# Performance work log

Measured on AMD Instinct MI355X. Metric: run time of the kernel, lower is better.

## Reference

```python
import jax, jax.numpy as jnp
import numpy as np

B, S, IN_D, OUT_D, QD = 4, 1024, 16, 16, 32
HID, HEADS, HD, L, TED = 256, 8, 32, 4, 256
DECAY = 0.1
SCALE = HD ** -0.5


def _ln(x):
    m = x.mean(-1, keepdims=True)
    v = ((x - m) ** 2).mean(-1, keepdims=True)
    return (x - m) * jax.lax.rsqrt(v + 1e-5)


def _lin(x, w, b):
    # torch nn.Linear: y = x @ W^T + b, W is [out, in]
    return jnp.einsum('...i,oi->...o', x, w) + b


def _sin_emb(t, dim):
    half = dim // 2
    freqs = jnp.exp(-np.log(10000.0) * jnp.arange(half, dtype=jnp.float32) / (half - 1))
    a = t[:, None] * freqs[None, :]
    return jnp.concatenate([jnp.sin(a), jnp.cos(a)], axis=-1)


def _mish(x):
    return x * jnp.tanh(jax.nn.softplus(x))


def _gelu(x):
    return jax.nn.gelu(x, approximate=False)


def setup_inputs() -> dict:
    key = jax.random.key(0)
    ks = iter(jax.random.split(key, 64))

    def w(shape):
        return jax.random.normal(next(ks), shape, dtype=jnp.float32) * 0.02

    d = {}
    d['x'] = jax.random.normal(next(ks), (B, S, IN_D), dtype=jnp.float32)
    d['query'] = jax.random.normal(next(ks), (B, QD), dtype=jnp.float32)
    d['time'] = jax.random.uniform(next(ks), (B,), dtype=jnp.float32) * 1000.0
    d['tm_w1'] = w((TED * 4, TED)); d['tm_b1'] = jnp.zeros((TED * 4,), jnp.float32)
    d['tm_w2'] = w((TED, TED * 4)); d['tm_b2'] = jnp.zeros((TED,), jnp.float32)
    d['in_w'] = w((HID, IN_D)); d['in_b'] = jnp.zeros((HID,), jnp.float32)
    d['q_w1'] = w((HID, QD)); d['q_b1'] = jnp.zeros((HID,), jnp.float32)
    d['q_w2'] = w((HID, HID)); d['q_b2'] = jnp.zeros((HID,), jnp.float32)
    d['n1_w'] = jnp.ones((L, HID), jnp.float32); d['n1_b'] = jnp.zeros((L, HID), jnp.float32)
    d['qkv_w'] = w((L, 3 * HID, HID)); d['qkv_b'] = jnp.zeros((L, 3 * HID), jnp.float32)
    d['ap_w'] = w((L, HID, HID)); d['ap_b'] = jnp.zeros((L, HID), jnp.float32)
    d['rel_bias'] = w((L, 2 * S - 1, HEADS))
    d['n2_w'] = jnp.ones((L, HID), jnp.float32); d['n2_b'] = jnp.zeros((L, HID), jnp.float32)
    d['f1_w'] = w((L, 4 * HID, HID)); d['f1_b'] = jnp.zeros((L, 4 * HID), jnp.float32)
    d['f2_w'] = w((L, HID, 4 * HID)); d['f2_b'] = jnp.zeros((L, HID), jnp.float32)
    d['t1_w'] = w((L, HID, TED)); d['t1_b'] = jnp.zeros((L, HID), jnp.float32)
    d['t2_w'] = w((L, HID, HID)); d['t2_b'] = jnp.zeros((L, HID), jnp.float32)
    d['out_w'] = w((OUT_D, HID)); d['out_b'] = jnp.zeros((OUT_D,), jnp.float32)
    return d


def reference(x, query, time, tm_w1, tm_b1, tm_w2, tm_b2, in_w, in_b,
              q_w1, q_b1, q_w2, q_b2, n1_w, n1_b, qkv_w, qkv_b, ap_w, ap_b,
              rel_bias, n2_w, n2_b, f1_w, f1_b, f2_w, f2_b, t1_w, t1_b,
              t2_w, t2_b, out_w, out_b):
    Bx, Sx, _ = x.shape
    # time MLP: SinusoidalPosEmb -> Linear -> Mish -> Linear
    te = _lin(_sin_emb(time, TED), tm_w1, tm_b1)
    te = _lin(_mish(te), tm_w2, tm_b2)            # [B, TED]
    # input projection + query conditioning (relative-pos path: no abs pos emb)
    h = _lin(x, in_w, in_b)                        # [B, S, HID]
    qe = _lin(_gelu(_lin(query, q_w1, q_b1)), q_w2, q_b2)
    h = h + qe[:, None, :]
    # shared relative-distance structures
    idx = jnp.arange(Sx)
    rel = idx[:, None] - idx[None, :]              # [S, S]
    dec = jnp.exp(-DECAY * jnp.abs(rel).astype(jnp.float32))
    rel_idx = rel + S - 1                          # index into 2*max_seq_len-1 table
    for l in range(L):
        # time conditioning per block
        tp = _lin(_gelu(_lin(te, t1_w[l], t1_b[l])), t2_w[l], t2_b[l])
        xn = _ln(h + tp[:, None, :]) * n1_w[l] + n1_b[l]
        qkv = _lin(xn, qkv_w[l], qkv_b[l]).reshape(Bx, Sx, 3, HEADS, HD)
        qkv = qkv.transpose(2, 0, 3, 1, 4)          # [3, B, H, S, hd]
        q_, k_, v_ = qkv[0], qkv[1], qkv[2]
        attn = jnp.einsum('bhqd,bhkd->bhqk', q_, k_) * SCALE
        bias = rel_bias[l][rel_idx]                 # [S, S, H]
        attn = attn + (dec[:, :, None] * bias).transpose(2, 0, 1)[None]
        a = jax.nn.softmax(attn, axis=-1)
        o = jnp.einsum('bhqk,bhkd->bhqd', a, v_)
        o = o.transpose(0, 2, 1, 3).reshape(Bx, Sx, HID)
        h = h + _lin(o, ap_w[l], ap_b[l])           # residual from pre-time x
        xn2 = _ln(h) * n2_w[l] + n2_b[l]
        h = h + _lin(_gelu(_lin(xn2, f1_w[l], f1_b[l])), f2_w[l], f2_b[l])
    return _lin(h, out_w, out_b)
```

## Files before the change

kernel.cpp:

```cpp
#include <hip/hip_runtime.h>
#include <hip/hip_bf16.h>
#include <math.h>

#define S_LEN 1024
#define HID 256
#define HEADS 8
#define HD 32
#define NLAYER 4
#define TED 256
#define BATCH 4
#define DECAY 0.1f
#define ATT_SCALE 0.17677669529663687f
#define LOG2E 1.4426950408889634f

typedef __bf16 bf8_t __attribute__((ext_vector_type(8)));
typedef float f4_t __attribute__((ext_vector_type(4)));

__device__ __forceinline__ float gelu_f(float x) {
  return 0.5f * x * (1.f + erff(x * 0.70710678118654752f));
}
__device__ __forceinline__ __bf16 f2bf(float f) { return (__bf16)f; }

__global__ __launch_bounds__(256) void k_prep_a(
    const float* __restrict__ timev,
    const float* __restrict__ tm_w1, const float* __restrict__ tm_b1,
    const float* __restrict__ query,
    const float* __restrict__ q_w1, const float* __restrict__ q_b1,
    float* __restrict__ te1, float* __restrict__ q1) {
  int bid = blockIdx.x;
  int lane = threadIdx.x & 63;
  if (bid < 1024) {
    int r = bid * 4 + (threadIdx.x >> 6);
    int o = r & 1023, b = r >> 10;
    float t = timev[b];
    float ev[4];
#pragma unroll
    for (int e = 0; e < 4; e++) {
      int k = lane * 4 + e;
      int i = k & 127;
      float f = __expf(-logf(10000.f) * (float)i / 127.f);
      float a = t * f;
      ev[e] = (k < 128) ? sinf(a) : cosf(a);
    }
    const float* w = tm_w1 + (size_t)o * 256 + lane * 4;
    float4 w4 = *(const float4*)w;
    float s = ev[0] * w4.x + ev[1] * w4.y + ev[2] * w4.z + ev[3] * w4.w;
#pragma unroll
    for (int off = 32; off; off >>= 1) s += __shfl_xor(s, off);
    if (lane == 0) {
      s += tm_b1[o];
      float sp = (s > 20.f) ? s : log1pf(__expf(s));
      te1[r] = s * tanhf(sp);
    }
  } else {
    int r = (bid - 1024) * 4 + (threadIdx.x >> 6);
    int o = r & 255, b = r >> 8;
    float s = 0.f;
    if (lane < 8) {
      float4 a4 = *(const float4*)(query + b * 32 + lane * 4);
      float4 w4 = *(const float4*)(q_w1 + (size_t)o * 32 + lane * 4);
      s = a4.x * w4.x + a4.y * w4.y + a4.z * w4.z + a4.w * w4.w;
    }
#pragma unroll
    for (int off = 32; off; off >>= 1) s += __shfl_xor(s, off);
    if (lane == 0) q1[r] = gelu_f(s + q_b1[o]);
  }
}

__global__ __launch_bounds__(256) void k_prep_b(
    const float* __restrict__ te1, const float* __restrict__ tm_w2,
    const float* __restrict__ tm_b2,
    const float* __restrict__ q1, const float* __restrict__ q_w2,
    const float* __restrict__ q_b2,
    float* __restrict__ te, float* __restrict__ qe) {
  int bid = blockIdx.x;
  int lane = threadIdx.x & 63;
  bool iste = bid < 256;
  int r = (iste ? bid : bid - 256) * 4 + (threadIdx.x >> 6);
  int o = r & 255, b = r >> 8;
  int K = iste ? 1024 : 256;
  const float* a = (iste ? te1 : q1) + (size_t)b * K;
  const float* w = (iste ? tm_w2 : q_w2) + (size_t)o * K;
  float s = 0.f;
  for (int k = lane * 4; k < K; k += 256) {
    float4 a4 = *(const float4*)(a + k);
    float4 w4 = *(const float4*)(w + k);
    s += a4.x * w4.x + a4.y * w4.y + a4.z * w4.z + a4.w * w4.w;
  }
#pragma unroll
  for (int off = 32; off; off >>= 1) s += __shfl_xor(s, off);
  if (lane == 0) {
    s += (iste ? tm_b2 : q_b2)[o];
    (iste ? te : qe)[r] = s;
  }
}

template <int ACT, bool APG>
__global__ __launch_bounds__(256) void k_gemv(
    const float* __restrict__ A, const float* __restrict__ W,
    const float* __restrict__ bias, float* __restrict__ out,
    int K, int OUT) {
  int r = blockIdx.x * 4 + (threadIdx.x >> 6);
  int lane = threadIdx.x & 63;
  int o = r % OUT;
  int b = (r / OUT) % BATCH;
  int g = r / (OUT * BATCH);
  const float* a = A + (size_t)((APG ? g * BATCH : 0) + b) * K;
  const float* w = W + (size_t)(g * OUT + o) * K;
  float s = 0.f;
  for (int k = lane * 4; k < K; k += 256) {
    float4 a4 = *(const float4*)(a + k);
    float4 w4 = *(const float4*)(w + k);
    s += a4.x * w4.x + a4.y * w4.y + a4.z * w4.z + a4.w * w4.w;
  }
#pragma unroll
  for (int off = 32; off; off >>= 1) s += __shfl_xor(s, off);
  if (lane == 0) {
    s += bias[g * OUT + o];
    if (ACT == 1) s = gelu_f(s);
    if (ACT == 2) {
      float sp = (s > 20.f) ? s : log1pf(__expf(s));
      s = s * tanhf(sp);
    }
    out[r] = s;
  }
}

__global__ __launch_bounds__(256) void k_inproj(
    const float* __restrict__ x, const float* __restrict__ in_w,
    const float* __restrict__ in_b, const float* __restrict__ qe,
    float* __restrict__ h) {
  int row = blockIdx.x;
  int b = row >> 10;
  int j = threadIdx.x;
  __shared__ float xr[16];
  if (j < 16) xr[j] = x[row * 16 + j];
  __syncthreads();
  float s = in_b[j] + qe[b * 256 + j];
  const float* w = in_w + j * 16;
#pragma unroll
  for (int i = 0; i < 16; i++) s += xr[i] * w[i];
  h[(size_t)row * 256 + j] = s;
}

__global__ __launch_bounds__(256) void k_cvtall(
    const float* __restrict__ s0, __bf16* __restrict__ d0,
    const float* __restrict__ s1, __bf16* __restrict__ d1,
    const float* __restrict__ s2, __bf16* __restrict__ d2,
    const float* __restrict__ s3, __bf16* __restrict__ d3,
    const float* __restrict__ relb, float* __restrict__ decb_t) {
  int bid = blockIdx.x;
  if (bid >= 1536) {
    int lb = bid - 1536;
    int l = lb >> 6;
    int i = (lb & 63) * 256 + threadIdx.x;
    if (i < 2047 * 8) {
      int idx = i >> 3, hh = i & 7;
      float dec = __expf(-DECAY * fabsf((float)(idx - 1023)));
      decb_t[(l * 8 + hh) * 2048 + idx] = dec * relb[(size_t)l * 2047 * 8 + i] * LOG2E;
    }
    return;
  }
  const float* s; __bf16* d; int base;
  if (bid < 384)       { s = s0; d = d0; base = bid; }
  else if (bid < 512)  { s = s1; d = d1; base = bid - 384; }
  else if (bid < 1024) { s = s2; d = d2; base = bid - 512; }
  else                 { s = s3; d = d3; base = bid - 1024; }
  int i = (base * 256 + threadIdx.x) * 8;
  float4 a = *(const float4*)(s + i);
  float4 b = *(const float4*)(s + i + 4);
  bf8_t o;
  o[0] = f2bf(a.x); o[1] = f2bf(a.y); o[2] = f2bf(a.z); o[3] = f2bf(a.w);
  o[4] = f2bf(b.x); o[5] = f2bf(b.y); o[6] = f2bf(b.z); o[7] = f2bf(b.w);
  *(bf8_t*)(d + i) = o;
}

template <int BN, int ACT, int OUTMODE, bool HASTP>
__global__ __launch_bounds__(256) void k_gemm_lnf(
    const float* __restrict__ h, const __bf16* __restrict__ W,
    const float* __restrict__ bias, void* __restrict__ Cv,
    const float* __restrict__ tp, const float* __restrict__ lw,
    const float* __restrict__ lb, int N) {
  constexpr int K = 256;
  constexpr int NJ = (BN / 2) / 16;
  constexpr int BQ = BN / 64;
  __shared__ __bf16 Al[64 * 264];
  __shared__ __bf16 Bl[2 * BN * 32];
  int tid = threadIdx.x;
  int w = tid >> 6, lane = tid & 63;
  int g = lane >> 4, c = lane & 15;
  int n0 = blockIdx.x * BN, m0 = blockIdx.y * 64;

  int srow = tid >> 2;
  int scol = (tid & 3) * 8;
  int sw = (((tid & 3) ^ ((tid >> 3) & 3))) * 8;
  const __bf16* Wb = W + (size_t)n0 * K + scol;
  bf8_t nB[2][BQ];
#pragma unroll
  for (int sub = 0; sub < 2; sub++)
#pragma unroll
    for (int q = 0; q < BQ; q++)
      nB[sub][q] = *(const bf8_t*)(Wb + (size_t)(q * 64 + srow) * K + sub * 32);

  int sub32 = tid & 31, lrow = tid >> 5;
  int colb = sub32 * 8;
  float4 lw0 = *(const float4*)(lw + colb), lw1 = *(const float4*)(lw + colb + 4);
  float4 lb0 = *(const float4*)(lb + colb), lb1 = *(const float4*)(lb + colb + 4);
  float4 tp0, tp1;
  if (HASTP) {
    const float* tpr = tp + (m0 >> 10) * 256 + colb;
    tp0 = *(const float4*)tpr; tp1 = *(const float4*)(tpr + 4);
  }
#pragma unroll
  for (int p = 0; p < 8; p++) {
    int row = p * 8 + lrow;
    const float* hr = h + (size_t)(m0 + row) * 256 + colb;
    float4 a = *(const float4*)hr;
    float4 b2 = *(const float4*)(hr + 4);
    if (HASTP) {
      a.x += tp0.x; a.y += tp0.y; a.z += tp0.z; a.w += tp0.w;
      b2.x += tp1.x; b2.y += tp1.y; b2.z += tp1.z; b2.w += tp1.w;
    }
    float sum = a.x + a.y + a.z + a.w + b2.x + b2.y + b2.z + b2.w;
    float ss = a.x * a.x + a.y * a.y + a.z * a.z + a.w * a.w +
               b2.x * b2.x + b2.y * b2.y + b2.z * b2.z + b2.w * b2.w;
#pragma unroll
    for (int m = 1; m < 32; m <<= 1) {
      sum += __shfl_xor(sum, m);
      ss += __shfl_xor(ss, m);
    }
    float mean = sum * (1.f / 256.f);
    float var = ss * (1.f / 256.f) - mean * mean;
    float rs = rsqrtf(var + 1e-5f);
    bf8_t o;
    o[0] = f2bf((a.x - mean) * rs * lw0.x + lb0.x);
    o[1] = f2bf((a.y - mean) * rs * lw0.y + lb0.y);
    o[2] = f2bf((a.z - mean) * rs * lw0.z + lb0.z);
    o[3] = f2bf((a.w - mean) * rs * lw0.w + lb0.w);
    o[4] = f2bf((b2.x - mean) * rs * lw1.x + lb1.x);
    o[5] = f2bf((b2.y - mean) * rs * lw1.y + lb1.y);
    o[6] = f2bf((b2.z - mean) * rs * lw1.z + lb1.z);
    o[7] = f2bf((b2.w - mean) * rs * lw1.w + lb1.w);
    *(bf8_t*)&Al[row * 264 + colb] = o;
  }

  int wr = (w >> 1) * 32, wc = (w & 1) * (BN / 2);
  int aseg = ((g ^ ((c >> 1) & 3))) * 8;
  f4_t acc[2][NJ];
#pragma unroll
  for (int i = 0; i < 2; i++)
#pragma unroll
    for (int j = 0; j < NJ; j++) acc[i][j] = (f4_t){0.f, 0.f, 0.f, 0.f};

#pragma unroll
  for (int ph = 0; ph < 4; ph++) {
    __syncthreads();
#pragma unroll
    for (int sub = 0; sub < 2; sub++)
#pragma unroll
      for (int q = 0; q < BQ; q++)
        *(bf8_t*)&Bl[sub * BN * 32 + (q * 64 + srow) * 32 + sw] = nB[sub][q];
    __syncthreads();
    if (ph < 3) {
#pragma unroll
      for (int sub = 0; sub < 2; sub++)
#pragma unroll
        for (int q = 0; q < BQ; q++)
          nB[sub][q] = *(const bf8_t*)(Wb + (size_t)(q * 64 + srow) * K +
                                       (ph + 1) * 64 + sub * 32);
    }
#pragma unroll
    for (int sub = 0; sub < 2; sub++) {
      bf8_t af[2], bfr[NJ];
#pragma unroll
      for (int i = 0; i < 2; i++)
        af[i] = *(const bf8_t*)&Al[(wr + i * 16 + c) * 264 + ph * 64 + sub * 32 + g * 8];
#pragma unroll
      for (int j = 0; j < NJ; j++)
        bfr[j] = *(const bf8_t*)&Bl[sub * BN * 32 + (wc + j * 16 + c) * 32 + aseg];
#pragma unroll
      for (int i = 0; i < 2; i++)
#pragma unroll
        for (int j = 0; j < NJ; j++)
          acc[i][j] = __builtin_amdgcn_mfma_f32_16x16x32_bf16(af[i], bfr[j], acc[i][j], 0, 0, 0);
    }
  }
#pragma unroll
  for (int j = 0; j < NJ; j++) {
    int col = n0 + wc + j * 16 + c;
    float bv = bias[col];
#pragma unroll
    for (int i = 0; i < 2; i++) {
#pragma unroll
      for (int rr = 0; rr < 4; rr++) {
        int row = m0 + wr + i * 16 + 4 * g + rr;
        float v = acc[i][j][rr] + bv;
        if (ACT == 1) v = gelu_f(v);
        size_t idx = (size_t)row * N + col;
        if (OUTMODE == 1) ((float*)Cv)[idx] += v;
        else ((__bf16*)Cv)[idx] = f2bf(v);
      }
    }
  }
}

__global__ __launch_bounds__(256) void k_attn(
    const __bf16* __restrict__ qkv, const float* __restrict__ decb_t,
    __bf16* __restrict__ obuf) {
  __shared__ __bf16 Kl[64 * 40];
  __shared__ __bf16 Vt[32 * 72];
  __shared__ __bf16 Pl[4][16 * 72];
  __shared__ float db[1088];

  int tid = threadIdx.x;
  int w = tid >> 6, lane = tid & 63;
  int g = lane >> 4, c = lane & 15;
  int bh = blockIdx.y;
  int b = bh >> 3, hh = bh & 7;
  int q0 = blockIdx.x * 64;

  for (int i = tid; i < 1087; i += 256) db[i] = decb_t[hh * 2048 + q0 + i];

  bf8_t qraw = *(const bf8_t*)(qkv + ((size_t)(b * S_LEN + q0 + w * 16 + c)) * 768 + hh * 32 + 8 * g);
  bf8_t qfrag;
#pragma unroll
  for (int i = 0; i < 8; i++) qfrag[i] = f2bf((float)qraw[i] * (ATT_SCALE * LOG2E));

  float ps_acc[4] = {0.f, 0.f, 0.f, 0.f};
  f4_t o0 = {0.f, 0.f, 0.f, 0.f}, o1 = {0.f, 0.f, 0.f, 0.f};

  int rowb = w * 16 + 4 * g;
  __bf16* Plw = &Pl[w][0];

  int kvr = tid & 63, part = tid >> 6;
  const __bf16* base0 = qkv + ((size_t)(b * S_LEN + kvr)) * 768 + hh * 32 + part * 8;
  bf8_t k8 = *(const bf8_t*)(base0 + 256);
  bf8_t v8 = *(const bf8_t*)(base0 + 512);

  for (int c0 = 0; c0 < S_LEN; c0 += 64) {
    __syncthreads();
    {
      *(bf8_t*)&Kl[kvr * 40 + part * 8] = k8;
      int d0s = part * 8;
#pragma unroll
      for (int jj = 0; jj < 8; jj++) Vt[(d0s + jj) * 72 + kvr] = v8[jj];
    }
    __syncthreads();
    if (c0 + 64 < S_LEN) {
      const __bf16* basen = base0 + (size_t)(c0 + 64) * 768;
      k8 = *(const bf8_t*)(basen + 256);
      v8 = *(const bf8_t*)(basen + 512);
    }

    f4_t sc[4];
    f4_t zero4 = {0.f, 0.f, 0.f, 0.f};
#pragma unroll
    for (int j = 0; j < 4; j++) {
      bf8_t kfrag = *(const bf8_t*)&Kl[(j * 16 + c) * 40 + g * 8];
      sc[j] = __builtin_amdgcn_mfma_f32_16x16x32_bf16(qfrag, kfrag, zero4, 0, 0, 0);
    }
#pragma unroll
    for (int j = 0; j < 4; j++) {
      int bidx = rowb + 1023 - (c0 + j * 16 + c);
#pragma unroll
      for (int r = 0; r < 4; r++) {
        float p = exp2f(sc[j][r] + db[bidx + r]);
        ps_acc[r] += p;
        Plw[(4 * g + r) * 72 + j * 16 + c] = f2bf(p);
      }
    }
#pragma unroll
    for (int ss = 0; ss < 2; ss++) {
      bf8_t pa = *(const bf8_t*)&Plw[c * 72 + ss * 32 + g * 8];
      bf8_t v0 = *(const bf8_t*)&Vt[c * 72 + ss * 32 + g * 8];
      bf8_t v1 = *(const bf8_t*)&Vt[(c + 16) * 72 + ss * 32 + g * 8];
      o0 = __builtin_amdgcn_mfma_f32_16x16x32_bf16(pa, v0, o0, 0, 0, 0);
      o1 = __builtin_amdgcn_mfma_f32_16x16x32_bf16(pa, v1, o1, 0, 0, 0);
    }
  }

#pragma unroll
  for (int r = 0; r < 4; r++) {
#pragma unroll
    for (int m = 1; m < 16; m <<= 1) ps_acc[r] += __shfl_xor(ps_acc[r], m);
    float inv = 1.f / ps_acc[r];
    size_t rowg = (size_t)(b * S_LEN + q0 + rowb + r);
    obuf[rowg * 256 + hh * 32 + c] = f2bf(o0[r] * inv);
    obuf[rowg * 256 + hh * 32 + 16 + c] = f2bf(o1[r] * inv);
  }
}

__global__ __launch_bounds__(512) void k_back(
    const __bf16* __restrict__ obb, float* __restrict__ h,
    const __bf16* __restrict__ wap, const float* __restrict__ apb,
    const float* __restrict__ n2w, const float* __restrict__ n2b,
    const __bf16* __restrict__ wf1, const float* __restrict__ f1b,
    const __bf16* __restrict__ wf2, const float* __restrict__ f2b) {
  __shared__ __bf16 Asm[16 * 264];
  __shared__ __bf16 Bl[2 * 256 * 32];
  __shared__ __bf16 y1l[16 * 1032];
  __shared__ float red[16][8][2];

  int tid = threadIdx.x;
  int w = tid >> 6, lane = tid & 63;
  int g = lane >> 4, c = lane & 15;
  int m0 = blockIdx.x * 16;
  int srow = tid >> 2;
  int scol = (tid & 3) * 8;
  int sw = (((tid & 3) ^ ((srow >> 1) & 3))) * 8;
  int wc = w * 32;
  int axor = (c >> 1) & 3;
  int boff0 = (wc + c) * 32 + ((g ^ axor)) * 8;
  int boff1 = (wc + 16 + c) * 32 + ((g ^ axor)) * 8;
  int col0 = wc + c, col1 = wc + 16 + c;
  f4_t zero4 = {0.f, 0.f, 0.f, 0.f};

  bf8_t nB[2][2];
  auto prefetch = [&](const __bf16* base, int K, int ko) {
#pragma unroll
    for (int s = 0; s < 2; s++)
#pragma unroll
      for (int q = 0; q < 2; q++)
        nB[s][q] = *(const bf8_t*)(base + (size_t)(q * 128 + srow) * K + ko + s * 32 + scol);
  };
  auto stageB = [&]() {
    __syncthreads();
#pragma unroll
    for (int s = 0; s < 2; s++)
#pragma unroll
      for (int q = 0; q < 2; q++)
        *(bf8_t*)&Bl[s * 8192 + (q * 128 + srow) * 32 + sw] = nB[s][q];
    __syncthreads();
  };
  f4_t a0, a1;
  auto mstep = [&](const __bf16* Ab, int AS, int ko) {
#pragma unroll
    for (int s = 0; s < 2; s++) {
      bf8_t af = *(const bf8_t*)&Ab[c * AS + ko + s * 32 + g * 8];
      bf8_t b0 = *(const bf8_t*)&Bl[s * 8192 + boff0];
      bf8_t b1 = *(const bf8_t*)&Bl[s * 8192 + boff1];
      a0 = __builtin_amdgcn_mfma_f32_16x16x32_bf16(af, b0, a0, 0, 0, 0);
      a1 = __builtin_amdgcn_mfma_f32_16x16x32_bf16(af, b1, a1, 0, 0, 0);
    }
  };

  prefetch(wap, 256, 0);
  {
    int row = tid >> 5, gr = tid & 31;
    *(bf8_t*)&Asm[row * 264 + gr * 8] = *(const bf8_t*)(obb + (size_t)(m0 + row) * 256 + gr * 8);
  }

  a0 = zero4; a1 = zero4;
#pragma unroll
  for (int ph = 0; ph < 4; ph++) {
    stageB();
    if (ph < 3) prefetch(wap, 256, (ph + 1) * 64);
    else prefetch(wf1, 256, 0);
    mstep(Asm, 264, ph * 64);
  }

  float hn[2][4];
  {
    float b0v = apb[col0], b1v = apb[col1];
    float ps[4], pq[4];
#pragma unroll
    for (int r = 0; r < 4; r++) {
      size_t row = (size_t)(m0 + 4 * g + r);
      float v0 = a0[r] + b0v + h[row * 256 + col0];
      float v1 = a1[r] + b1v + h[row * 256 + col1];
      h[row * 256 + col0] = v0;
      h[row * 256 + col1] = v1;
      hn[0][r] = v0; hn[1][r] = v1;
      ps[r] = v0 + v1;
      pq[r] = v0 * v0 + v1 * v1;
    }
#pragma unroll
    for (int r = 0; r < 4; r++) {
#pragma unroll
      for (int m = 1; m < 16; m <<= 1) {
        ps[r] += __shfl_xor(ps[r], m);
        pq[r] += __shfl_xor(pq[r], m);
      }
    }
    if (c == 0) {
#pragma unroll
      for (int r = 0; r < 4; r++) {
        red[4 * g + r][w][0] = ps[r];
        red[4 * g + r][w][1] = pq[r];
      }
    }
  }
  __syncthreads();
  {
    float n2w0 = n2w[col0], n2b0 = n2b[col0];
    float n2w1 = n2w[col1], n2b1 = n2b[col1];
#pragma unroll
    for (int r = 0; r < 4; r++) {
      int row = 4 * g + r;
      float S = 0.f, Q = 0.f;
#pragma unroll
      for (int ww = 0; ww < 8; ww++) { S += red[row][ww][0]; Q += red[row][ww][1]; }
      float mean = S * (1.f / 256.f);
      float var = Q * (1.f / 256.f) - mean * mean;
      float rs = rsqrtf(var + 1e-5f);
      Asm[row * 264 + col0] = f2bf((hn[0][r] - mean) * rs * n2w0 + n2b0);
      Asm[row * 264 + col1] = f2bf((hn[1][r] - mean) * rs * n2w1 + n2b1);
    }
  }

#pragma unroll
  for (int nc = 0; nc < 4; nc++) {
    a0 = zero4; a1 = zero4;
#pragma unroll
    for (int ph = 0; ph < 4; ph++) {
      stageB();
      if (ph < 3) prefetch(wf1 + nc * 65536, 256, (ph + 1) * 64);
      else if (nc < 3) prefetch(wf1 + (nc + 1) * 65536, 256, 0);
      else prefetch(wf2, 1024, 0);
      mstep(Asm, 264, ph * 64);
    }
    float b0v = f1b[nc * 256 + col0], b1v = f1b[nc * 256 + col1];
#pragma unroll
    for (int r = 0; r < 4; r++) {
      y1l[(4 * g + r) * 1032 + nc * 256 + col0] = f2bf(gelu_f(a0[r] + b0v));
      y1l[(4 * g + r) * 1032 + nc * 256 + col1] = f2bf(gelu_f(a1[r] + b1v));
    }
  }

  a0 = zero4; a1 = zero4;
#pragma unroll
  for (int ph = 0; ph < 16; ph++) {
    stageB();
    if (ph < 15) prefetch(wf2, 1024, (ph + 1) * 64);
    mstep(y1l, 1032, ph * 64);
  }
  {
    float b0v = f2b[col0], b1v = f2b[col1];
#pragma unroll
    for (int r = 0; r < 4; r++) {
      size_t row = (size_t)(m0 + 4 * g + r);
      h[row * 256 + col0] += a0[r] + b0v;
      h[row * 256 + col1] += a1[r] + b1v;
    }
  }
}

__global__ __launch_bounds__(256) void k_out(
    const float* __restrict__ hbuf, const float* __restrict__ out_w,
    const float* __restrict__ out_b, float* __restrict__ out) {
  int tid = threadIdx.x;
  int r = blockIdx.x * 16 + (tid >> 4);
  int c = tid & 15;
  const float4* hr = (const float4*)(hbuf + (size_t)r * 256);
  const float4* w4 = (const float4*)(out_w + c * 256);
  float s = out_b[c];
#pragma unroll 8
  for (int k = 0; k < 64; k++) {
    float4 a = hr[k], b = w4[k];
    s += a.x * b.x + a.y * b.y + a.z * b.z + a.w * b.w;
  }
  out[r * 16 + c] = s;
}

extern "C" void kernel_launch(void* const* d_in, const int* in_sizes, int n_in,
                              void* d_out, int out_size, void* d_ws, size_t ws_size,
                              hipStream_t stream) {
  const float* x      = (const float*)d_in[0];
  const float* query  = (const float*)d_in[1];
  const float* timev  = (const float*)d_in[2];
  const float* tm_w1  = (const float*)d_in[3];
  const float* tm_b1  = (const float*)d_in[4];
  const float* tm_w2  = (const float*)d_in[5];
  const float* tm_b2  = (const float*)d_in[6];
  const float* in_w   = (const float*)d_in[7];
  const float* in_b   = (const float*)d_in[8];
  const float* q_w1   = (const float*)d_in[9];
  const float* q_b1   = (const float*)d_in[10];
  const float* q_w2   = (const float*)d_in[11];
  const float* q_b2   = (const float*)d_in[12];
  const float* n1_w   = (const float*)d_in[13];
  const float* n1_b   = (const float*)d_in[14];
  const float* qkv_w  = (const float*)d_in[15];
  const float* qkv_b  = (const float*)d_in[16];
  const float* ap_w   = (const float*)d_in[17];
  const float* ap_b   = (const float*)d_in[18];
  const float* relb   = (const float*)d_in[19];
  const float* n2_w   = (const float*)d_in[20];
  const float* n2_b   = (const float*)d_in[21];
  const float* f1_w   = (const float*)d_in[22];
  const float* f1_b   = (const float*)d_in[23];
  const float* f2_w   = (const float*)d_in[24];
  const float* f2_b   = (const float*)d_in[25];
  const float* t1_w   = (const float*)d_in[26];
  const float* t1_b   = (const float*)d_in[27];
  const float* t2_w   = (const float*)d_in[28];
  const float* t2_b   = (const float*)d_in[29];
  const float* out_w  = (const float*)d_in[30];
  const float* out_b  = (const float*)d_in[31];
  float* out = (float*)d_out;

  float* ws = (float*)d_ws;
  float*  h    = ws;
  __bf16* qkvb = (__bf16*)(ws + 1572864);
  __bf16* obb  = (__bf16*)(ws + 3145728);
  __bf16* wqkv = (__bf16*)(ws + 5767168);
  __bf16* wap  = (__bf16*)(ws + 6160384);
  __bf16* wf1  = (__bf16*)(ws + 6291456);
  __bf16* wf2  = (__bf16*)(ws + 6815744);
  float* decb  = ws + 7340032;
  float* qe    = decb + 65536;
  float* tp    = qe + 1024;
  float* te1   = tp + 4096;
  float* te    = te1 + 4096;
  float* q1    = te + 1024;
  float* tt    = q1 + 1024;

  k_cvtall<<<1792, 256, 0, stream>>>(qkv_w, wqkv, ap_w, wap, f1_w, wf1, f2_w, wf2,
                                     relb, decb);

  k_prep_a<<<1280, 256, 0, stream>>>(timev, tm_w1, tm_b1, query, q_w1, q_b1, te1, q1);
  k_prep_b<<<512, 256, 0, stream>>>(te1, tm_w2, tm_b2, q1, q_w2, q_b2, te, qe);
  k_gemv<1, false><<<1024, 256, 0, stream>>>(te, t1_w, t1_b, tt, 256, 256);
  k_gemv<0, true><<<1024, 256, 0, stream>>>(tt, t2_w, t2_b, tp, 256, 256);

  k_inproj<<<4096, 256, 0, stream>>>(x, in_w, in_b, qe, h);

  for (int l = 0; l < NLAYER; l++) {
    k_gemm_lnf<128, 0, 2, true><<<dim3(6, 64), 256, 0, stream>>>(
        h, wqkv + (size_t)l * 196608, qkv_b + l * 768, qkvb,
        tp + l * 1024, n1_w + l * 256, n1_b + l * 256, 768);
    k_attn<<<dim3(16, 32), 256, 0, stream>>>(qkvb, decb + l * 16384, obb);
    k_back<<<256, 512, 0, stream>>>(
        obb, h, wap + (size_t)l * 65536, ap_b + l * 256,
        n2_w + l * 256, n2_b + l * 256,
        wf1 + (size_t)l * 262144, f1_b + l * 1024,
        wf2 + (size_t)l * 262144, f2_b + l * 256);
  }
  k_out<<<256, 256, 0, stream>>>(h, out_w, out_b, out);
}
```

Before: 282.7 us.

## Widen attention KV tile to 128, add MFMA priority hints, merge prep kernels

The attention kernel now processes 128 keys per iteration instead of 64. This halves the number of barrier-synchronised tile loads and doubles the MFMA work done between syncs, and s_setprio raises wave priority around the MFMA sections. Separately, the weight-conversion and first prep kernels are merged into one launch, as are the time-MLP first GEMV and the input projection, which removes launch overhead. The larger tiles raise LDS use (Kl, Vt, Pl) and register pressure from sc[8], which may reduce occupancy.

```diff
diff --git a/kernel.cpp b/kernel.cpp
--- a/kernel.cpp
+++ b/kernel.cpp
@@ -21,7 +21,12 @@
 }
 __device__ __forceinline__ __bf16 f2bf(float f) { return (__bf16)f; }
 
-__global__ __launch_bounds__(256) void k_prep_a(
+__global__ __launch_bounds__(256) void k_boot(
+    const float* __restrict__ s0, __bf16* __restrict__ d0,
+    const float* __restrict__ s1, __bf16* __restrict__ d1,
+    const float* __restrict__ s2, __bf16* __restrict__ d2,
+    const float* __restrict__ s3, __bf16* __restrict__ d3,
+    const float* __restrict__ relb, float* __restrict__ decb_t,
     const float* __restrict__ timev,
     const float* __restrict__ tm_w1, const float* __restrict__ tm_b1,
     const float* __restrict__ query,
@@ -29,8 +34,30 @@
     float* __restrict__ te1, float* __restrict__ q1) {
   int bid = blockIdx.x;
   int lane = threadIdx.x & 63;
-  if (bid < 1024) {
-    int r = bid * 4 + (threadIdx.x >> 6);
+  if (bid < 1536) {
+    const float* s; __bf16* d; int base;
+    if (bid < 384)       { s = s0; d = d0; base = bid; }
+    else if (bid < 512)  { s = s1; d = d1; base = bid - 384; }
+    else if (bid < 1024) { s = s2; d = d2; base = bid - 512; }
+    else                 { s = s3; d = d3; base = bid - 1024; }
+    int i = (base * 256 + threadIdx.x) * 8;
+    float4 a = *(const float4*)(s + i);
+    float4 b = *(const float4*)(s + i + 4);
+    bf8_t o;
+    o[0] = f2bf(a.x); o[1] = f2bf(a.y); o[2] = f2bf(a.z); o[3] = f2bf(a.w);
+    o[4] = f2bf(b.x); o[5] = f2bf(b.y); o[6] = f2bf(b.z); o[7] = f2bf(b.w);
+    *(bf8_t*)(d + i) = o;
+  } else if (bid < 1792) {
+    int lb = bid - 1536;
+    int l = lb >> 6;
+    int i = (lb & 63) * 256 + threadIdx.x;
+    if (i < 2047 * 8) {
+      int idx = i >> 3, hh = i & 7;
+      float dec = __expf(-DECAY * fabsf((float)(idx - 1023)));
+      decb_t[(l * 8 + hh) * 2048 + idx] = dec * relb[(size_t)l * 2047 * 8 + i] * LOG2E;
+    }
+  } else if (bid < 2816) {
+    int r = (bid - 1792) * 4 + (threadIdx.x >> 6);
     int o = r & 1023, b = r >> 10;
     float t = timev[b];
     float ev[4];
@@ -42,8 +69,7 @@
       float a = t * f;
       ev[e] = (k < 128) ? sinf(a) : cosf(a);
     }
-    const float* w = tm_w1 + (size_t)o * 256 + lane * 4;
-    float4 w4 = *(const float4*)w;
+    float4 w4 = *(const float4*)(tm_w1 + (size_t)o * 256 + lane * 4);
     float s = ev[0] * w4.x + ev[1] * w4.y + ev[2] * w4.z + ev[3] * w4.w;
 #pragma unroll
     for (int off = 32; off; off >>= 1) s += __shfl_xor(s, off);
@@ -53,7 +79,7 @@
       te1[r] = s * tanhf(sp);
     }
   } else {
-    int r = (bid - 1024) * 4 + (threadIdx.x >> 6);
+    int r = (bid - 2816) * 4 + (threadIdx.x >> 6);
     int o = r & 255, b = r >> 8;
     float s = 0.f;
     if (lane < 8) {
@@ -95,6 +121,45 @@
   }
 }
 
+__global__ __launch_bounds__(256) void k_mid(
+    const float* __restrict__ te, const float* __restrict__ t1_w,
+    const float* __restrict__ t1_b, float* __restrict__ tt,
+    const float* __restrict__ x, const float* __restrict__ in_w,
+    const float* __restrict__ in_b, const float* __restrict__ qe,
+    float* __restrict__ h) {
+  int bid = blockIdx.x;
+  if (bid < 1024) {
+    int r = bid * 4 + (threadIdx.x >> 6);
+    int lane = threadIdx.x & 63;
+    int o = r & 255;
+    int b = (r >> 8) & 3;
+    int g = r >> 10;
+    const float* a = te + (size_t)b * 256;
+    const float* w = t1_w + ((size_t)(g * 256 + o)) * 256;
+    float s = 0.f;
+    for (int k = lane * 4; k < 256; k += 256) {
+      float4 a4 = *(const float4*)(a + k);
+      float4 w4 = *(const float4*)(w + k);
+      s += a4.x * w4.x + a4.y * w4.y + a4.z * w4.z + a4.w * w4.w;
+    }
+#pragma unroll
+    for (int off = 32; off; off >>= 1) s += __shfl_xor(s, off);
+    if (lane == 0) tt[r] = gelu_f(s + t1_b[g * 256 + o]);
+  } else {
+    int row = bid - 1024;
+    int b = row >> 10;
+    int j = threadIdx.x;
+    __shared__ float xr[16];
+    if (j < 16) xr[j] = x[row * 16 + j];
+    __syncthreads();
+    float s = in_b[j] + qe[b * 256 + j];
+    const float* w = in_w + j * 16;
+#pragma unroll
+    for (int i = 0; i < 16; i++) s += xr[i] * w[i];
+    h[(size_t)row * 256 + j] = s;
+  }
+}
+
 template <int ACT, bool APG>
 __global__ __launch_bounds__(256) void k_gemv(
     const float* __restrict__ A, const float* __restrict__ W,
@@ -126,55 +191,6 @@
   }
 }
 
-__global__ __launch_bounds__(256) void k_inproj(
-    const float* __restrict__ x, const float* __restrict__ in_w,
-    const float* __restrict__ in_b, const float* __restrict__ qe,
-    float* __restrict__ h) {
-  int row = blockIdx.x;
-  int b = row >> 10;
-  int j = threadIdx.x;
-  __shared__ float xr[16];
-  if (j < 16) xr[j] = x[row * 16 + j];
-  __syncthreads();
-  float s = in_b[j] + qe[b * 256 + j];
-  const float* w = in_w + j * 16;
-#pragma unroll
-  for (int i = 0; i < 16; i++) s += xr[i] * w[i];
-  h[(size_t)row * 256 + j] = s;
-}
-
-__global__ __launch_bounds__(256) void k_cvtall(
-    const float* __restrict__ s0, __bf16* __restrict__ d0,
-    const float* __restrict__ s1, __bf16* __restrict__ d1,
-    const float* __restrict__ s2, __bf16* __restrict__ d2,
-    const float* __restrict__ s3, __bf16* __restrict__ d3,
-    const float* __restrict__ relb, float* __restrict__ decb_t) {
-  int bid = blockIdx.x;
-  if (bid >= 1536) {
-    int lb = bid - 1536;
-    int l = lb >> 6;
-    int i = (lb & 63) * 256 + threadIdx.x;
-    if (i < 2047 * 8) {
-      int idx = i >> 3, hh = i & 7;
-      float dec = __expf(-DECAY * fabsf((float)(idx - 1023)));
-      decb_t[(l * 8 + hh) * 2048 + idx] = dec * relb[(size_t)l * 2047 * 8 + i] * LOG2E;
-    }
-    return;
-  }
-  const float* s; __bf16* d; int base;
-  if (bid < 384)       { s = s0; d = d0; base = bid; }
-  else if (bid < 512)  { s = s1; d = d1; base = bid - 384; }
-  else if (bid < 1024) { s = s2; d = d2; base = bid - 512; }
-  else                 { s = s3; d = d3; base = bid - 1024; }
-  int i = (base * 256 + threadIdx.x) * 8;
-  float4 a = *(const float4*)(s + i);
-  float4 b = *(const float4*)(s + i + 4);
-  bf8_t o;
-  o[0] = f2bf(a.x); o[1] = f2bf(a.y); o[2] = f2bf(a.z); o[3] = f2bf(a.w);
-  o[4] = f2bf(b.x); o[5] = f2bf(b.y); o[6] = f2bf(b.z); o[7] = f2bf(b.w);
-  *(bf8_t*)(d + i) = o;
-}
-
 template <int BN, int ACT, int OUTMODE, bool HASTP>
 __global__ __launch_bounds__(256) void k_gemm_lnf(
     const float* __restrict__ h, const __bf16* __restrict__ W,
@@ -307,9 +323,9 @@
 __global__ __launch_bounds__(256) void k_attn(
     const __bf16* __restrict__ qkv, const float* __restrict__ decb_t,
     __bf16* __restrict__ obuf) {
-  __shared__ __bf16 Kl[64 * 40];
-  __shared__ __bf16 Vt[32 * 72];
-  __shared__ __bf16 Pl[4][16 * 72];
+  __shared__ __bf16 Kl[128 * 40];
+  __shared__ __bf16 Vt[32 * 136];
+  __shared__ __bf16 Pl[4][16 * 136];
   __shared__ float db[1088];
 
   int tid = threadIdx.x;
@@ -332,51 +348,63 @@
   int rowb = w * 16 + 4 * g;
   __bf16* Plw = &Pl[w][0];
 
-  int kvr = tid & 63, part = tid >> 6;
-  const __bf16* base0 = qkv + ((size_t)(b * S_LEN + kvr)) * 768 + hh * 32 + part * 8;
-  bf8_t k8 = *(const bf8_t*)(base0 + 256);
-  bf8_t v8 = *(const bf8_t*)(base0 + 512);
-
-  for (int c0 = 0; c0 < S_LEN; c0 += 64) {
+  int kvr = tid & 127;
+  int part = tid >> 7;
+  const __bf16* base0 = qkv + ((size_t)(b * S_LEN + kvr)) * 768 + hh * 32 + part * 16;
+  bf8_t k8a = *(const bf8_t*)(base0 + 256);
+  bf8_t k8b = *(const bf8_t*)(base0 + 264);
+  bf8_t v8a = *(const bf8_t*)(base0 + 512);
+  bf8_t v8b = *(const bf8_t*)(base0 + 520);
+
+  for (int c0 = 0; c0 < S_LEN; c0 += 128) {
     __syncthreads();
     {
-      *(bf8_t*)&Kl[kvr * 40 + part * 8] = k8;
-      int d0s = part * 8;
-#pragma unroll
-      for (int jj = 0; jj < 8; jj++) Vt[(d0s + jj) * 72 + kvr] = v8[jj];
+      *(bf8_t*)&Kl[kvr * 40 + part * 16] = k8a;
+      *(bf8_t*)&Kl[kvr * 40 + part * 16 + 8] = k8b;
+      int d0s = part * 16;
+#pragma unroll
+      for (int jj = 0; jj < 8; jj++) Vt[(d0s + jj) * 136 + kvr] = v8a[jj];
+#pragma unroll
+      for (int jj = 0; jj < 8; jj++) Vt[(d0s + 8 + jj) * 136 + kvr] = v8b[jj];
     }
     __syncthreads();
-    if (c0 + 64 < S_LEN) {
-      const __bf16* basen = base0 + (size_t)(c0 + 64) * 768;
-      k8 = *(const bf8_t*)(basen + 256);
-      v8 = *(const bf8_t*)(basen + 512);
-    }
-
-    f4_t sc[4];
+    if (c0 + 128 < S_LEN) {
+      const __bf16* basen = base0 + (size_t)(c0 + 128) * 768;
+      k8a = *(const bf8_t*)(basen + 256);
+      k8b = *(const bf8_t*)(basen + 264);
+      v8a = *(const bf8_t*)(basen + 512);
+      v8b = *(const bf8_t*)(basen + 520);
+    }
+
+    f4_t sc[8];
     f4_t zero4 = {0.f, 0.f, 0.f, 0.f};
-#pragma unroll
-    for (int j = 0; j < 4; j++) {
+    __builtin_amdgcn_s_setprio(1);
+#pragma unroll
+    for (int j = 0; j < 8; j++) {
       bf8_t kfrag = *(const bf8_t*)&Kl[(j * 16 + c) * 40 + g * 8];
       sc[j] = __builtin_amdgcn_mfma_f32_16x16x32_bf16(qfrag, kfrag, zero4, 0, 0, 0);
     }
-#pragma unroll
-    for (int j = 0; j < 4; j++) {
+    __builtin_amdgcn_s_setprio(0);
+#pragma unroll
+    for (int j = 0; j < 8; j++) {
       int bidx = rowb + 1023 - (c0 + j * 16 + c);
 #pragma unroll
       for (int r = 0; r < 4; r++) {
         float p = exp2f(sc[j][r] + db[bidx + r]);
         ps_acc[r] += p;
-        Plw[(4 * g + r) * 72 + j * 16 + c] = f2bf(p);
+        Plw[(4 * g + r) * 136 + j * 16 + c] = f2bf(p);
       }
     }
-#pragma unroll
-    for (int ss = 0; ss < 2; ss++) {
-      bf8_t pa = *(const bf8_t*)&Plw[c * 72 + ss * 32 + g * 8];
-      bf8_t v0 = *(const bf8_t*)&Vt[c * 72 + ss * 32 + g * 8];
-      bf8_t v1 = *(const bf8_t*)&Vt[(c + 16) * 72 + ss * 32 + g * 8];
+    __builtin_amdgcn_s_setprio(1);
+#pragma unroll
+    for (int ss = 0; ss < 4; ss++) {
+      bf8_t pa = *(const bf8_t*)&Plw[c * 136 + ss * 32 + g * 8];
+      bf8_t v0 = *(const bf8_t*)&Vt[c * 136 + ss * 32 + g * 8];
+      bf8_t v1 = *(const bf8_t*)&Vt[(c + 16) * 136 + ss * 32 + g * 8];
       o0 = __builtin_amdgcn_mfma_f32_16x16x32_bf16(pa, v0, o0, 0, 0, 0);
       o1 = __builtin_amdgcn_mfma_f32_16x16x32_bf16(pa, v1, o1, 0, 0, 0);
     }
+    __builtin_amdgcn_s_setprio(0);
   }
 
 #pragma unroll
@@ -615,15 +643,12 @@
   float* q1    = te + 1024;
   float* tt    = q1 + 1024;
 
-  k_cvtall<<<1792, 256, 0, stream>>>(qkv_w, wqkv, ap_w, wap, f1_w, wf1, f2_w, wf2,
-                                     relb, decb);
-
-  k_prep_a<<<1280, 256, 0, stream>>>(timev, tm_w1, tm_b1, query, q_w1, q_b1, te1, q1);
+  k_boot<<<3072, 256, 0, stream>>>(qkv_w, wqkv, ap_w, wap, f1_w, wf1, f2_w, wf2,
+                                   relb, decb, timev, tm_w1, tm_b1,
+                                   query, q_w1, q_b1, te1, q1);
   k_prep_b<<<512, 256, 0, stream>>>(te1, tm_w2, tm_b2, q1, q_w2, q_b2, te, qe);
-  k_gemv<1, false><<<1024, 256, 0, stream>>>(te, t1_w, t1_b, tt, 256, 256);
+  k_mid<<<5120, 256, 0, stream>>>(te, t1_w, t1_b, tt, x, in_w, in_b, qe, h);
   k_gemv<0, true><<<1024, 256, 0, stream>>>(tt, t2_w, t2_b, tp, 256, 256);
-
-  k_inproj<<<4096, 256, 0, stream>>>(x, in_w, in_b, qe, h);
 
   for (int l = 0; l < NLAYER; l++) {
     k_gemm_lnf<128, 0, 2, true><<<dim3(6, 64), 256, 0, stream>>>(
```

Result: no change. 279.8 us (-1.0%).
